# Kernel optimization log

Measured on AMD Instinct MI355X. Metric: run time of the kernel, lower is better.

Reference implementation:

```python
import jax, jax.numpy as jnp
import numpy as np

B, S, D, H = 2, 2048, 1024, 16
DK = D // H

def setup_inputs() -> dict:
    key = jax.random.key(0)
    ks = jax.random.split(key, 12)
    scale = 1.0 / np.sqrt(D)
    inp = {
        'q': jax.random.normal(ks[0], (B, S, D), jnp.float32),
        'k': jax.random.normal(ks[1], (B, S, D), jnp.float32),
        'v': jax.random.normal(ks[2], (B, S, D), jnp.float32),
        # causal mask: 1 where attending is allowed (j <= i), 0 for future tokens
        'mask': jnp.tril(jnp.ones((S, S), jnp.int32))[None, None, :, :],
        'wq': jax.random.normal(ks[3], (D, D), jnp.float32) * scale,
        'bq': jnp.zeros((D,), jnp.float32),
        'wk': jax.random.normal(ks[4], (D, D), jnp.float32) * scale,
        'bk': jnp.zeros((D,), jnp.float32),
        'wv': jax.random.normal(ks[5], (D, D), jnp.float32) * scale,
        'bv': jnp.zeros((D,), jnp.float32),
        'wo': jax.random.normal(ks[6], (D, D), jnp.float32) * scale,
        'bo': jnp.zeros((D,), jnp.float32),
    }
    return inp


def reference(q, k, v, mask, wq, bq, wk, bk, wv, bv, wo, bo):
    def split_heads(x):
        # [B,S,D] -> [B,H,S,DK]
        return x.reshape(B, S, H, DK).transpose(0, 2, 1, 3)

    query = split_heads(q @ wq + bq)
    key_ = split_heads(k @ wk + bk)
    value = split_heads(v @ wv + bv)

    # [B,H,S,S] attention scores
    scores = jnp.einsum('bhqd,bhkd->bhqk', query, key_) / jnp.sqrt(
        jnp.asarray(DK, jnp.float32))
    scores = jnp.where(mask == 0, jnp.asarray(-1e9, scores.dtype), scores)
    attn = jax.nn.softmax(scores, axis=-1)  # dropout p=0.0 (eval mode)

    x = jnp.einsum('bhqk,bhkd->bhqd', attn, value)  # [B,H,S,DK]
    x = x.transpose(0, 2, 1, 3).reshape(B, S, D)
    return x @ wo + bo
```

## Files before the change

### kernel.cpp

```cpp
#include <hip/hip_runtime.h>
#include <hip/hip_bf16.h>

#define BATCH 2
#define SEQ   2048
#define DMODEL 1024
#define NHEAD 16
#define DK    64
#define MTOK  (BATCH * SEQ)

typedef __attribute__((ext_vector_type(8))) short bf16x8;
typedef __attribute__((ext_vector_type(4))) float f32x4;

__device__ __forceinline__ unsigned short f2bf(float x) {
    unsigned u = __float_as_uint(x);
    u = (u + 0x7FFFu + ((u >> 16) & 1u)) >> 16;
    return (unsigned short)u;
}

__device__ __forceinline__ void store_out(float* p, float v)          { *p = v; }
__device__ __forceinline__ void store_out(unsigned short* p, float v) { *p = f2bf(v); }

__device__ __forceinline__ unsigned cvt_pk_bf16(float x, float y) {
    unsigned d;
    asm("v_cvt_pk_bf16_f32 %0, %1, %2" : "=v"(d) : "v"(x), "v"(y));
    return d;
}

__device__ __forceinline__ void g2lds16(const void* g, void* l) {
    __builtin_amdgcn_global_load_lds(
        (const __attribute__((address_space(1))) void*)g,
        (__attribute__((address_space(3))) void*)l, 16, 0, 0);
}

template <int N>
__device__ __forceinline__ void s_wait_vmcnt() {
    asm volatile("s_waitcnt vmcnt(%0)" :: "n"(N) : "memory");
}
__device__ __forceinline__ void s_wait_lgkm0() {
    asm volatile("s_waitcnt lgkmcnt(0)" ::: "memory");
}
__device__ __forceinline__ void s_bar() {
    asm volatile("s_barrier" ::: "memory");
}

__global__ __launch_bounds__(256) void cvt3_bf16_kernel(
    const float* __restrict__ s0, const float* __restrict__ s1,
    const float* __restrict__ s2,
    unsigned short* __restrict__ d0, unsigned short* __restrict__ d1,
    unsigned short* __restrict__ d2, int n)
{
    const float* src; unsigned short* dst;
    switch (blockIdx.z) {
        case 0:  src = s0; dst = d0; break;
        case 1:  src = s1; dst = d1; break;
        default: src = s2; dst = d2; break;
    }
    int i = (blockIdx.x * 256 + threadIdx.x) * 8;
    if (i >= n) return;
    float4 a = *(const float4*)(src + i);
    float4 b = *(const float4*)(src + i + 4);
    union { unsigned short s[8]; uint4 u; } o;
    o.s[0] = f2bf(a.x); o.s[1] = f2bf(a.y); o.s[2] = f2bf(a.z); o.s[3] = f2bf(a.w);
    o.s[4] = f2bf(b.x); o.s[5] = f2bf(b.y); o.s[6] = f2bf(b.z); o.s[7] = f2bf(b.w);
    *(uint4*)(dst + i) = o.u;
}

__global__ __launch_bounds__(256) void wtrans_kernel(
    const float* __restrict__ w0, const float* __restrict__ w1,
    const float* __restrict__ w2, const float* __restrict__ w3,
    unsigned short* __restrict__ t0, unsigned short* __restrict__ t1,
    unsigned short* __restrict__ t2, unsigned short* __restrict__ t3)
{
    __shared__ float tile[32][33];
    const float* W; unsigned short* T;
    switch (blockIdx.z) {
        case 0:  W = w0; T = t0; break;
        case 1:  W = w1; T = t1; break;
        case 2:  W = w2; T = t2; break;
        default: W = w3; T = t3; break;
    }
    const int n0 = blockIdx.x * 32, k0 = blockIdx.y * 32;
    const int t  = threadIdx.x;
    const int r  = t >> 3;
    const int c4 = (t & 7) * 4;

    float4 v = *(const float4*)&W[(size_t)(k0 + r) * DMODEL + n0 + c4];
    tile[r][c4 + 0] = v.x; tile[r][c4 + 1] = v.y;
    tile[r][c4 + 2] = v.z; tile[r][c4 + 3] = v.w;
    __syncthreads();

    union { unsigned short s[4]; uint2 u; } o;
#pragma unroll
    for (int u = 0; u < 4; ++u) o.s[u] = f2bf(tile[c4 + u][r]);
    *(uint2*)&T[(size_t)(n0 + r) * DMODEL + k0 + c4] = o.u;
}

struct GemmP {
    const unsigned short* A;
    const unsigned short* Bt;
    const float* bias;
    void* C;
    int N, K, ctShift, biasByRow;
    float scale;
};
struct Gemm3 { GemmP p[3]; };

template <typename OutT, int MR, int NC>
__global__ __launch_bounds__(512, 2) void gemm_lds_kernel(Gemm3 g)
{
    constexpr int AM    = MR / 2;
    constexpr int NCW   = NC / 4;
    constexpr int NBLK  = 2 * MR + 2 * NC;
    constexpr int PW    = NBLK / 8;
    constexpr int BUFSZ = NBLK * 512;

    __shared__ unsigned short sS[2 * BUFSZ];

    const unsigned nx  = gridDim.x;
    const unsigned lin = blockIdx.x + nx * blockIdx.z;
    const unsigned ch  = (nx * gridDim.z) >> 3;
    const unsigned l2  = (lin & 7u) * ch + (lin >> 3);
    const unsigned zz  = l2 / nx;
    const unsigned bid = l2 - zz * nx;

    const GemmP p = g.p[zz];
    const unsigned short* __restrict__ A  = p.A;
    const unsigned short* __restrict__ Bt = p.Bt;
    OutT* __restrict__ C = (OutT*)p.C;
    const int K = p.K, N = p.N;

    const int bx = (int)(bid & ((1u << p.ctShift) - 1u));
    const int by = (int)(bid >> p.ctShift);
    const int row0 = by * (MR * 16);
    const int col0 = bx * (NC * 16);

    const int t    = threadIdx.x;
    const int w    = t >> 6;
    const int lane = t & 63;
    const int ln   = lane & 15;
    const int qg   = lane >> 4;
    const int wm   = w >> 2;
    const int wn   = w & 3;

    const unsigned short* sp[PW];
    int lo[PW];
#pragma unroll
    for (int i = 0; i < PW; ++i) {
        const int s = w * PW + i;
        if (s < 2 * MR) {
            const int mtg = s >> 1, kc = s & 1;
            sp[i] = A + (size_t)(row0 + mtg * 16 + ln) * K + kc * 32 + qg * 8;
        } else {
            const int bi = s - 2 * MR;
            const int ntg = bi >> 1, kc = bi & 1;
            sp[i] = Bt + (size_t)(col0 + ntg * 16 + ln) * K + kc * 32 + qg * 8;
        }
        lo[i] = s * 512;
    }

    f32x4 acc[AM][NCW];
#pragma unroll
    for (int mt = 0; mt < AM; ++mt)
#pragma unroll
        for (int nt = 0; nt < NCW; ++nt) acc[mt][nt] = (f32x4){0.f, 0.f, 0.f, 0.f};

    const int NT = K / 64;

#pragma unroll
    for (int i = 0; i < PW; ++i) g2lds16(sp[i], &sS[lo[i]]);
#pragma unroll
    for (int i = 0; i < PW; ++i) g2lds16(sp[i] + 64, &sS[BUFSZ + lo[i]]);

    int curOff = 0;
    for (int kt = 0; kt < NT; ++kt) {
        if (kt < NT - 1) s_wait_vmcnt<PW>();
        else             s_wait_vmcnt<0>();
        s_bar();

        const unsigned short* bufA = &sS[curOff];
        const unsigned short* bufB = &sS[curOff + 2 * MR * 512];
#pragma unroll
        for (int kc = 0; kc < 2; ++kc) {
            bf16x8 aF[AM], bF[NCW];
#pragma unroll
            for (int mt = 0; mt < AM; ++mt)
                aF[mt] = *(const bf16x8*)&bufA[(((wm * AM + mt) * 2) + kc) * 512 + lane * 8];
#pragma unroll
            for (int n2 = 0; n2 < NCW; ++n2)
                bF[n2] = *(const bf16x8*)&bufB[(((wn * NCW + n2) * 2) + kc) * 512 + lane * 8];
#pragma unroll
            for (int mt = 0; mt < AM; ++mt)
#pragma unroll
                for (int n2 = 0; n2 < NCW; ++n2)
                    acc[mt][n2] = __builtin_amdgcn_mfma_f32_16x16x32_bf16(
                        aF[mt], bF[n2], acc[mt][n2], 0, 0, 0);
        }

        s_wait_lgkm0();
        s_bar();

        if (kt + 2 < NT) {
            const int koff = (kt + 2) * 64;
#pragma unroll
            for (int i = 0; i < PW; ++i)
                g2lds16(sp[i] + koff, &sS[curOff + lo[i]]);
        }
        curOff ^= BUFSZ;
    }

    float bcol[NCW], brow[AM][4];
    if (!p.biasByRow) {
#pragma unroll
        for (int n2 = 0; n2 < NCW; ++n2)
            bcol[n2] = p.bias[col0 + (wn * NCW + n2) * 16 + ln];
    } else {
#pragma unroll
        for (int mt = 0; mt < AM; ++mt)
#pragma unroll
            for (int r = 0; r < 4; ++r)
                brow[mt][r] = p.bias[row0 + wm * (AM * 16) + mt * 16 + qg * 4 + r];
    }

#pragma unroll
    for (int mt = 0; mt < AM; ++mt)
#pragma unroll
        for (int n2 = 0; n2 < NCW; ++n2)
#pragma unroll
            for (int r = 0; r < 4; ++r) {
                int row = row0 + wm * (AM * 16) + mt * 16 + qg * 4 + r;
                int col = col0 + (wn * NCW + n2) * 16 + ln;
                float bb = p.biasByRow ? brow[mt][r] : bcol[n2];
                store_out(&C[(size_t)row * N + col], (acc[mt][n2][r] + bb) * p.scale);
            }
}

#define BR 64
#define BC 64

__global__ __launch_bounds__(256) void attn_mfma_kernel(
    const unsigned short* __restrict__ Qg, const unsigned short* __restrict__ Kg,
    const unsigned short* __restrict__ VT, unsigned short* __restrict__ O)
{
    __shared__ unsigned short sK[2][8 * 512];
    __shared__ unsigned short sV[2][8 * 512];
    __shared__ unsigned short sQ[8 * 512];

    const int t    = threadIdx.x;
    const int w    = t >> 6;
    const int lane = t & 63;
    const int ln   = lane & 15;
    const int qg   = lane >> 4;

    const int id  = blockIdx.x;
    const int bh  = id & 31;
    const int qt  = (SEQ / BR - 1) - (id >> 5);
    const int b   = bh >> 4;
    const int h   = bh & 15;
    const int qi0 = qt * BR;

    const size_t rowbase = (size_t)b * SEQ;
    const size_t colbase = (size_t)h * DK;

#pragma unroll
    for (int i = 0; i < 2; ++i) {
        const int s = w * 2 + i;
        const int nt = s >> 1, kc = s & 1;
        g2lds16(Qg + (rowbase + qi0 + w * 16 + ln) * DMODEL + colbase + i * 32 + qg * 8,
                &sQ[s * 512]);
        g2lds16(Kg + (rowbase + nt * 16 + ln) * DMODEL + colbase + kc * 32 + qg * 8,
                &sK[0][s * 512]);
        g2lds16(VT + (size_t)(colbase + nt * 16 + ln) * MTOK + rowbase + kc * 32 + qg * 8,
                &sV[0][s * 512]);
    }
    __syncthreads();

    bf16x8 aq[2];
#pragma unroll
    for (int kc = 0; kc < 2; ++kc)
        aq[kc] = *(const bf16x8*)&sQ[(w * 2 + kc) * 512 + lane * 8];

    f32x4 ofrag[4];
#pragma unroll
    for (int nt = 0; nt < 4; ++nt) ofrag[nt] = (f32x4){0.f, 0.f, 0.f, 0.f};
    float osum_p = 0.f;
    float m_run  = -3.0e38f;

    const int laneA = ((2 * qg) & 3) * 16 + ln;
    const int laneB = ((2 * qg + 1) & 3) * 16 + ln;
    const bool hiSel = (qg >> 1) & 1;

    const int ntiles = qt + 1;
    for (int jt = 0; jt < ntiles; ++jt) {
        const int cur = jt & 1;

        if (jt + 1 < ntiles) {
            const int j1 = (jt + 1) * BC;
            const int nb = cur ^ 1;
#pragma unroll
            for (int i = 0; i < 2; ++i) {
                const int s = w * 2 + i;
                const int nt = s >> 1, kc = s & 1;
                g2lds16(Kg + (rowbase + j1 + nt * 16 + ln) * DMODEL + colbase + kc * 32 + qg * 8,
                        &sK[nb][s * 512]);
                g2lds16(VT + (size_t)(colbase + nt * 16 + ln) * MTOK + rowbase + j1 + kc * 32 + qg * 8,
                        &sV[nb][s * 512]);
            }
        }

        f32x4 sf[4];
#pragma unroll
        for (int nt = 0; nt < 4; ++nt) {
            f32x4 a2 = (f32x4){0.f, 0.f, 0.f, 0.f};
#pragma unroll
            for (int kc = 0; kc < 2; ++kc) {
                bf16x8 bk = *(const bf16x8*)&sK[cur][(nt * 2 + kc) * 512 + lane * 8];
                a2 = __builtin_amdgcn_mfma_f32_16x16x32_bf16(bk, aq[kc], a2, 0, 0, 0);
            }
            sf[nt] = a2;
        }

        if (jt == ntiles - 1) {
            const int qloc = w * 16 + ln;
#pragma unroll
            for (int nt = 0; nt < 4; ++nt)
#pragma unroll
                for (int r = 0; r < 4; ++r)
                    if (nt * 16 + qg * 4 + r > qloc) sf[nt][r] = -1.0e30f;
        }

        float pmax = sf[0][0];
#pragma unroll
        for (int nt = 0; nt < 4; ++nt)
#pragma unroll
            for (int r = 0; r < 4; ++r) pmax = fmaxf(pmax, sf[nt][r]);
        pmax = fmaxf(pmax, __shfl_xor(pmax, 16));
        pmax = fmaxf(pmax, __shfl_xor(pmax, 32));

        const float mn = fmaxf(m_run, pmax);
        const float al = exp2f(m_run - mn);
        m_run = mn;

        float pv[4][4];
        float lsum = 0.f;
#pragma unroll
        for (int nt = 0; nt < 4; ++nt)
#pragma unroll
            for (int r = 0; r < 4; ++r) {
                float e = exp2f(sf[nt][r] - mn);
                pv[nt][r] = e;
                lsum += e;
            }
        osum_p = osum_p * al + lsum;

        float alr[4];
#pragma unroll
        for (int r = 0; r < 4; ++r) alr[r] = __shfl(al, qg * 4 + r);
#pragma unroll
        for (int nt = 0; nt < 4; ++nt)
#pragma unroll
            for (int r = 0; r < 4; ++r) ofrag[nt][r] *= alr[r];

        unsigned pk0[2], pk1[2], pk2[2], pk3[2];
#pragma unroll
        for (int rr = 0; rr < 2; ++rr) {
            pk0[rr] = cvt_pk_bf16(pv[0][2 * rr], pv[0][2 * rr + 1]);
            pk1[rr] = cvt_pk_bf16(pv[1][2 * rr], pv[1][2 * rr + 1]);
            pk2[rr] = cvt_pk_bf16(pv[2][2 * rr], pv[2][2 * rr + 1]);
            pk3[rr] = cvt_pk_bf16(pv[3][2 * rr], pv[3][2 * rr + 1]);
        }
        union { bf16x8 v; unsigned u[4]; } ap[2];
        {
            unsigned s0, s1;
            s0 = (unsigned)__shfl((int)pk0[0], laneA); s1 = (unsigned)__shfl((int)pk1[0], laneA);
            ap[0].u[0] = hiSel ? s1 : s0;
            s0 = (unsigned)__shfl((int)pk0[1], laneA); s1 = (unsigned)__shfl((int)pk1[1], laneA);
            ap[0].u[1] = hiSel ? s1 : s0;
            s0 = (unsigned)__shfl((int)pk0[0], laneB); s1 = (unsigned)__shfl((int)pk1[0], laneB);
            ap[0].u[2] = hiSel ? s1 : s0;
            s0 = (unsigned)__shfl((int)pk0[1], laneB); s1 = (unsigned)__shfl((int)pk1[1], laneB);
            ap[0].u[3] = hiSel ? s1 : s0;
            s0 = (unsigned)__shfl((int)pk2[0], laneA); s1 = (unsigned)__shfl((int)pk3[0], laneA);
            ap[1].u[0] = hiSel ? s1 : s0;
            s0 = (unsigned)__shfl((int)pk2[1], laneA); s1 = (unsigned)__shfl((int)pk3[1], laneA);
            ap[1].u[1] = hiSel ? s1 : s0;
            s0 = (unsigned)__shfl((int)pk2[0], laneB); s1 = (unsigned)__shfl((int)pk3[0], laneB);
            ap[1].u[2] = hiSel ? s1 : s0;
            s0 = (unsigned)__shfl((int)pk2[1], laneB); s1 = (unsigned)__shfl((int)pk3[1], laneB);
            ap[1].u[3] = hiSel ? s1 : s0;
        }

#pragma unroll
        for (int nt = 0; nt < 4; ++nt) {
#pragma unroll
            for (int kc = 0; kc < 2; ++kc) {
                bf16x8 bv = *(const bf16x8*)&sV[cur][(nt * 2 + kc) * 512 + lane * 8];
                ofrag[nt] = __builtin_amdgcn_mfma_f32_16x16x32_bf16(ap[kc].v, bv, ofrag[nt], 0, 0, 0);
            }
        }

        __syncthreads();
    }

    float osum = osum_p + __shfl_xor(osum_p, 16);
    osum += __shfl_xor(osum, 32);
    const float invq = 1.0f / osum;
    float inv[4];
#pragma unroll
    for (int r = 0; r < 4; ++r) inv[r] = __shfl(invq, qg * 4 + r);
#pragma unroll
    for (int nt = 0; nt < 4; ++nt)
#pragma unroll
        for (int r = 0; r < 4; ++r) {
            int gq = qi0 + w * 16 + qg * 4 + r;
            O[(rowbase + gq) * DMODEL + colbase + nt * 16 + ln] =
                f2bf(ofrag[nt][r] * inv[r]);
        }
}

extern "C" void kernel_launch(void* const* d_in, const int* in_sizes, int n_in,
                              void* d_out, int out_size, void* d_ws, size_t ws_size,
                              hipStream_t stream)
{
    const float* q  = (const float*)d_in[0];
    const float* k  = (const float*)d_in[1];
    const float* v  = (const float*)d_in[2];
    const float* wq = (const float*)d_in[4];
    const float* bq = (const float*)d_in[5];
    const float* wk = (const float*)d_in[6];
    const float* bk = (const float*)d_in[7];
    const float* wv = (const float*)d_in[8];
    const float* bv = (const float*)d_in[9];
    const float* wo = (const float*)d_in[10];
    const float* bo = (const float*)d_in[11];
    float* out = (float*)d_out;

    const size_t mat  = (size_t)MTOK * DMODEL;
    const size_t wmat = (size_t)DMODEL * DMODEL;
    unsigned short* Abq = (unsigned short*)d_ws;
    unsigned short* Abk = Abq + mat;
    unsigned short* Abv = Abk + mat;
    unsigned short* WtQ = Abv + mat;
    unsigned short* WtK = WtQ + wmat;
    unsigned short* WtV = WtK + wmat;
    unsigned short* WtO = WtV + wmat;
    unsigned short* Qb  = WtO + wmat;
    unsigned short* Kb  = Qb + mat;
    unsigned short* VT  = Kb + mat;
    unsigned short* CTX = VT + mat;

    cvt3_bf16_kernel<<<dim3((unsigned)(mat / 2048), 1, 3), 256, 0, stream>>>(
        q, k, v, Abq, Abk, Abv, (int)mat);
    wtrans_kernel<<<dim3(32, 32, 4), 256, 0, stream>>>(wq, wk, wv, wo, WtQ, WtK, WtV, WtO);

    const float qscale = 0.125f * 1.44269504088896f;
    Gemm3 g;
    g.p[0] = (GemmP){Abq, WtQ, bq, (void*)Qb, DMODEL, DMODEL, 2, 0, qscale};
    g.p[1] = (GemmP){Abk, WtK, bk, (void*)Kb, DMODEL, DMODEL, 2, 0, 1.0f};
    g.p[2] = (GemmP){WtV, Abv, bv, (void*)VT, MTOK,   DMODEL, 4, 1, 1.0f};
    gemm_lds_kernel<unsigned short, 16, 16><<<dim3(64, 1, 3), 512, 0, stream>>>(g);

    attn_mfma_kernel<<<BATCH * NHEAD * (SEQ / BR), 256, 0, stream>>>(Qb, Kb, VT, CTX);

    Gemm3 go;
    go.p[0] = (GemmP){CTX, WtO, bo, (void*)out, DMODEL, DMODEL, 3, 0, 1.0f};
    go.p[1] = go.p[0];
    go.p[2] = go.p[0];
    gemm_lds_kernel<float, 8, 8><<<dim3(256, 1, 1), 512, 0, stream>>>(go);
}
```

Measured before the change: 257.1 us.

## Pipeline GEMM at half-tile (k=32) granularity with four-stage prefetch and MFMA priority

The GEMM main loop now advances in k=32 half-steps instead of k=64. Each half-slot of the double buffer is refilled as soon as it is consumed, so four half-tiles are in flight and the graduated vmcnt waits allow finer overlap of global-to-LDS loads with MFMA work. It also raises wave priority around the MFMA block with s_setprio. The cost is twice as many barriers per K and smaller compute chunks between them, which may offset the gain from better latency hiding.

```diff
diff --git a/kernel.cpp b/kernel.cpp
--- a/kernel.cpp
+++ b/kernel.cpp
@@ -110,9 +110,8 @@
 {
     constexpr int AM    = MR / 2;
     constexpr int NCW   = NC / 4;
-    constexpr int NBLK  = 2 * MR + 2 * NC;
-    constexpr int PW    = NBLK / 8;
-    constexpr int BUFSZ = NBLK * 512;
+    constexpr int HL    = (MR + NC) / 8;
+    constexpr int BUFSZ = (2 * MR + 2 * NC) * 512;
 
     __shared__ unsigned short sS[2 * BUFSZ];
 
@@ -142,20 +141,21 @@
     const int wm   = w >> 2;
     const int wn   = w & 3;
 
-    const unsigned short* sp[PW];
-    int lo[PW];
-#pragma unroll
-    for (int i = 0; i < PW; ++i) {
-        const int s = w * PW + i;
-        if (s < 2 * MR) {
-            const int mtg = s >> 1, kc = s & 1;
-            sp[i] = A + (size_t)(row0 + mtg * 16 + ln) * K + kc * 32 + qg * 8;
+    const unsigned short* sp[HL];
+    int d0[HL];
+    int dk[HL];
+#pragma unroll
+    for (int i = 0; i < HL; ++i) {
+        const int j = w * HL + i;
+        if (j < MR) {
+            sp[i] = A + (size_t)(row0 + j * 16 + ln) * K + qg * 8;
+            d0[i] = j * 512;
+            dk[i] = MR * 512;
         } else {
-            const int bi = s - 2 * MR;
-            const int ntg = bi >> 1, kc = bi & 1;
-            sp[i] = Bt + (size_t)(col0 + ntg * 16 + ln) * K + kc * 32 + qg * 8;
-        }
-        lo[i] = s * 512;
+            sp[i] = Bt + (size_t)(col0 + (j - MR) * 16 + ln) * K + qg * 8;
+            d0[i] = (2 * MR + (j - MR)) * 512;
+            dk[i] = NC * 512;
+        }
     }
 
     f32x4 acc[AM][NCW];
@@ -164,48 +164,54 @@
 #pragma unroll
         for (int nt = 0; nt < NCW; ++nt) acc[mt][nt] = (f32x4){0.f, 0.f, 0.f, 0.f};
 
-    const int NT = K / 64;
-
-#pragma unroll
-    for (int i = 0; i < PW; ++i) g2lds16(sp[i], &sS[lo[i]]);
-#pragma unroll
-    for (int i = 0; i < PW; ++i) g2lds16(sp[i] + 64, &sS[BUFSZ + lo[i]]);
-
-    int curOff = 0;
-    for (int kt = 0; kt < NT; ++kt) {
-        if (kt < NT - 1) s_wait_vmcnt<PW>();
-        else             s_wait_vmcnt<0>();
+    const int NH = K / 32;
+
+#pragma unroll
+    for (int hh = 0; hh < 4; ++hh) {
+        const int hb = (hh & 2) ? BUFSZ : 0;
+        const int kc = hh & 1;
+#pragma unroll
+        for (int i = 0; i < HL; ++i)
+            g2lds16(sp[i] + hh * 32, &sS[hb + d0[i] + kc * dk[i]]);
+    }
+
+    for (int h = 0; h < NH; ++h) {
+        if      (h + 3 < NH) s_wait_vmcnt<3 * HL>();
+        else if (h + 2 < NH) s_wait_vmcnt<2 * HL>();
+        else if (h + 1 < NH) s_wait_vmcnt<1 * HL>();
+        else                 s_wait_vmcnt<0>();
         s_bar();
 
-        const unsigned short* bufA = &sS[curOff];
-        const unsigned short* bufB = &sS[curOff + 2 * MR * 512];
-#pragma unroll
-        for (int kc = 0; kc < 2; ++kc) {
-            bf16x8 aF[AM], bF[NCW];
-#pragma unroll
-            for (int mt = 0; mt < AM; ++mt)
-                aF[mt] = *(const bf16x8*)&bufA[(((wm * AM + mt) * 2) + kc) * 512 + lane * 8];
+        const int hb = (h & 2) ? BUFSZ : 0;
+        const int kc = h & 1;
+        const unsigned short* bufA = &sS[hb + kc * (MR * 512)];
+        const unsigned short* bufB = &sS[hb + 2 * MR * 512 + kc * (NC * 512)];
+
+        bf16x8 aF[AM], bF[NCW];
+#pragma unroll
+        for (int mt = 0; mt < AM; ++mt)
+            aF[mt] = *(const bf16x8*)&bufA[(wm * AM + mt) * 512 + lane * 8];
+#pragma unroll
+        for (int n2 = 0; n2 < NCW; ++n2)
+            bF[n2] = *(const bf16x8*)&bufB[(wn * NCW + n2) * 512 + lane * 8];
+
+        __builtin_amdgcn_s_setprio(1);
+#pragma unroll
+        for (int mt = 0; mt < AM; ++mt)
 #pragma unroll
             for (int n2 = 0; n2 < NCW; ++n2)
-                bF[n2] = *(const bf16x8*)&bufB[(((wn * NCW + n2) * 2) + kc) * 512 + lane * 8];
-#pragma unroll
-            for (int mt = 0; mt < AM; ++mt)
-#pragma unroll
-                for (int n2 = 0; n2 < NCW; ++n2)
-                    acc[mt][n2] = __builtin_amdgcn_mfma_f32_16x16x32_bf16(
-                        aF[mt], bF[n2], acc[mt][n2], 0, 0, 0);
-        }
+                acc[mt][n2] = __builtin_amdgcn_mfma_f32_16x16x32_bf16(
+                    aF[mt], bF[n2], acc[mt][n2], 0, 0, 0);
+        __builtin_amdgcn_s_setprio(0);
 
         s_wait_lgkm0();
         s_bar();
 
-        if (kt + 2 < NT) {
-            const int koff = (kt + 2) * 64;
-#pragma unroll
-            for (int i = 0; i < PW; ++i)
-                g2lds16(sp[i] + koff, &sS[curOff + lo[i]]);
-        }
-        curOff ^= BUFSZ;
+        if (h + 4 < NH) {
+#pragma unroll
+            for (int i = 0; i < HL; ++i)
+                g2lds16(sp[i] + (h + 4) * 32, &sS[hb + d0[i] + kc * dk[i]]);
+        }
     }
 
     float bcol[NCW], brow[AM][4];
```

Measured after the change: 256.4 us. Within noise of the previous version (-0.2%).

## Split GEMM main loop into quadrant phases with barriers and MFMA priority

Applied to the files above, without the earlier changes.

Reworks the LDS-staged GEMM K-loop into four quadrant sub-phases (A-lo/B-lo, A-lo/B-hi, A-hi/B-lo, A-hi/B-hi). Fragment loads from LDS are interleaved with MFMA bursts, and the MFMA bursts are fenced by workgroup barriers and raised wave priority. The global prefetch moves from two tiles ahead to one tile ahead, issued at the start of each iteration, with a full vmcnt wait at the end. The aim is to overlap LDS reads with matrix math across waves in a ping-pong style. In exchange it adds many barriers and gives less lookahead to hide global-load latency.

```diff
diff --git a/kernel.cpp b/kernel.cpp
--- a/kernel.cpp
+++ b/kernel.cpp
@@ -110,6 +110,8 @@
 {
     constexpr int AM    = MR / 2;
     constexpr int NCW   = NC / 4;
+    constexpr int AMH   = AM / 2;
+    constexpr int NCWH  = NCW / 2;
     constexpr int NBLK  = 2 * MR + 2 * NC;
     constexpr int PW    = NBLK / 8;
     constexpr int BUFSZ = NBLK * 512;
@@ -168,44 +170,100 @@
 
 #pragma unroll
     for (int i = 0; i < PW; ++i) g2lds16(sp[i], &sS[lo[i]]);
-#pragma unroll
-    for (int i = 0; i < PW; ++i) g2lds16(sp[i] + 64, &sS[BUFSZ + lo[i]]);
-
-    int curOff = 0;
+    s_wait_vmcnt<0>();
+    s_bar();
+
     for (int kt = 0; kt < NT; ++kt) {
-        if (kt < NT - 1) s_wait_vmcnt<PW>();
-        else             s_wait_vmcnt<0>();
-        s_bar();
-
-        const unsigned short* bufA = &sS[curOff];
-        const unsigned short* bufB = &sS[curOff + 2 * MR * 512];
-#pragma unroll
-        for (int kc = 0; kc < 2; ++kc) {
-            bf16x8 aF[AM], bF[NCW];
-#pragma unroll
-            for (int mt = 0; mt < AM; ++mt)
-                aF[mt] = *(const bf16x8*)&bufA[(((wm * AM + mt) * 2) + kc) * 512 + lane * 8];
-#pragma unroll
-            for (int n2 = 0; n2 < NCW; ++n2)
-                bF[n2] = *(const bf16x8*)&bufB[(((wn * NCW + n2) * 2) + kc) * 512 + lane * 8];
-#pragma unroll
-            for (int mt = 0; mt < AM; ++mt)
-#pragma unroll
-                for (int n2 = 0; n2 < NCW; ++n2)
+        const int boff = (kt & 1) ? BUFSZ : 0;
+        const unsigned short* bufA = &sS[boff];
+        const unsigned short* bufB = &sS[boff + 2 * MR * 512];
+
+        bf16x8 aLo[AMH][2], aHi[AMH][2], bLo[NCWH][2], bHi[NCWH][2];
+
+        if (kt + 1 < NT) {
+            const int koff = (kt + 1) * 64;
+            const int doff = boff ^ BUFSZ;
+#pragma unroll
+            for (int i = 0; i < PW; ++i)
+                g2lds16(sp[i] + koff, &sS[doff + lo[i]]);
+        }
+#pragma unroll
+        for (int mt = 0; mt < AMH; ++mt)
+#pragma unroll
+            for (int kc = 0; kc < 2; ++kc)
+                aLo[mt][kc] = *(const bf16x8*)&bufA[((wm * AM + mt) * 2 + kc) * 512 + lane * 8];
+#pragma unroll
+        for (int n2 = 0; n2 < NCWH; ++n2)
+#pragma unroll
+            for (int kc = 0; kc < 2; ++kc)
+                bLo[n2][kc] = *(const bf16x8*)&bufB[((wn * NCW + n2) * 2 + kc) * 512 + lane * 8];
+        s_bar();
+        s_wait_lgkm0();
+        __builtin_amdgcn_sched_barrier(0);
+        __builtin_amdgcn_s_setprio(1);
+#pragma unroll
+        for (int mt = 0; mt < AMH; ++mt)
+#pragma unroll
+            for (int n2 = 0; n2 < NCWH; ++n2)
+#pragma unroll
+                for (int kc = 0; kc < 2; ++kc)
                     acc[mt][n2] = __builtin_amdgcn_mfma_f32_16x16x32_bf16(
-                        aF[mt], bF[n2], acc[mt][n2], 0, 0, 0);
-        }
-
+                        aLo[mt][kc], bLo[n2][kc], acc[mt][n2], 0, 0, 0);
+        __builtin_amdgcn_s_setprio(0);
+        s_bar();
+
+#pragma unroll
+        for (int n2 = 0; n2 < NCWH; ++n2)
+#pragma unroll
+            for (int kc = 0; kc < 2; ++kc)
+                bHi[n2][kc] = *(const bf16x8*)&bufB[((wn * NCW + NCWH + n2) * 2 + kc) * 512 + lane * 8];
+        s_bar();
         s_wait_lgkm0();
-        s_bar();
-
-        if (kt + 2 < NT) {
-            const int koff = (kt + 2) * 64;
-#pragma unroll
-            for (int i = 0; i < PW; ++i)
-                g2lds16(sp[i] + koff, &sS[curOff + lo[i]]);
-        }
-        curOff ^= BUFSZ;
+        __builtin_amdgcn_sched_barrier(0);
+        __builtin_amdgcn_s_setprio(1);
+#pragma unroll
+        for (int mt = 0; mt < AMH; ++mt)
+#pragma unroll
+            for (int n2 = 0; n2 < NCWH; ++n2)
+#pragma unroll
+                for (int kc = 0; kc < 2; ++kc)
+                    acc[mt][NCWH + n2] = __builtin_amdgcn_mfma_f32_16x16x32_bf16(
+                        aLo[mt][kc], bHi[n2][kc], acc[mt][NCWH + n2], 0, 0, 0);
+        __builtin_amdgcn_s_setprio(0);
+        s_bar();
+
+#pragma unroll
+        for (int mt = 0; mt < AMH; ++mt)
+#pragma unroll
+            for (int kc = 0; kc < 2; ++kc)
+                aHi[mt][kc] = *(const bf16x8*)&bufA[((wm * AM + AMH + mt) * 2 + kc) * 512 + lane * 8];
+        s_bar();
+        s_wait_lgkm0();
+        __builtin_amdgcn_sched_barrier(0);
+        __builtin_amdgcn_s_setprio(1);
+#pragma unroll
+        for (int mt = 0; mt < AMH; ++mt)
+#pragma unroll
+            for (int n2 = 0; n2 < NCWH; ++n2)
+#pragma unroll
+                for (int kc = 0; kc < 2; ++kc)
+                    acc[AMH + mt][n2] = __builtin_amdgcn_mfma_f32_16x16x32_bf16(
+                        aHi[mt][kc], bLo[n2][kc], acc[AMH + mt][n2], 0, 0, 0);
+        __builtin_amdgcn_s_setprio(0);
+        s_bar();
+
+        __builtin_amdgcn_s_setprio(1);
+#pragma unroll
+        for (int mt = 0; mt < AMH; ++mt)
+#pragma unroll
+            for (int n2 = 0; n2 < NCWH; ++n2)
+#pragma unroll
+                for (int kc = 0; kc < 2; ++kc)
+                    acc[AMH + mt][NCWH + n2] = __builtin_amdgcn_mfma_f32_16x16x32_bf16(
+                        aHi[mt][kc], bHi[n2][kc], acc[AMH + mt][NCWH + n2], 0, 0, 0);
+        __builtin_amdgcn_s_setprio(0);
+        s_wait_vmcnt<0>();
+        s_bar();
     }
 
     float bcol[NCW], brow[AM][4];
```

Result: slower. 266.3 us (+3.6%).

## Fuse fp32-to-bf16 activation conversion into QKV GEMM load pipeline

Applied to the files above, without the earlier changes.

Removes the separate cvt3 kernel that converted q/k/v activations to bf16 in workspace. The QKV GEMM now loads the fp32 activation tiles straight into registers, converts them with v_cvt_pk_bf16, and writes them to LDS, while the bf16 weight tiles still arrive by direct global-to-LDS loads. This avoids a full write and re-read of three activation matrices plus a kernel launch. In exchange the GEMM reads twice as many bytes for the A side, adds register pressure, and places a vmcnt wait and conversion step in the main loop. It also adds s_setprio around the MFMA block.

```diff
diff --git a/kernel.cpp b/kernel.cpp
--- a/kernel.cpp
+++ b/kernel.cpp
@@ -41,28 +41,6 @@
 }
 __device__ __forceinline__ void s_bar() {
     asm volatile("s_barrier" ::: "memory");
-}
-
-__global__ __launch_bounds__(256) void cvt3_bf16_kernel(
-    const float* __restrict__ s0, const float* __restrict__ s1,
-    const float* __restrict__ s2,
-    unsigned short* __restrict__ d0, unsigned short* __restrict__ d1,
-    unsigned short* __restrict__ d2, int n)
-{
-    const float* src; unsigned short* dst;
-    switch (blockIdx.z) {
-        case 0:  src = s0; dst = d0; break;
-        case 1:  src = s1; dst = d1; break;
-        default: src = s2; dst = d2; break;
-    }
-    int i = (blockIdx.x * 256 + threadIdx.x) * 8;
-    if (i >= n) return;
-    float4 a = *(const float4*)(src + i);
-    float4 b = *(const float4*)(src + i + 4);
-    union { unsigned short s[8]; uint4 u; } o;
-    o.s[0] = f2bf(a.x); o.s[1] = f2bf(a.y); o.s[2] = f2bf(a.z); o.s[3] = f2bf(a.w);
-    o.s[4] = f2bf(b.x); o.s[5] = f2bf(b.y); o.s[6] = f2bf(b.z); o.s[7] = f2bf(b.w);
-    *(uint4*)(dst + i) = o.u;
 }
 
 __global__ __launch_bounds__(256) void wtrans_kernel(
@@ -98,20 +76,24 @@
 struct GemmP {
     const unsigned short* A;
     const unsigned short* Bt;
+    const float* A32;
+    const float* B32;
     const float* bias;
     void* C;
-    int N, K, ctShift, biasByRow;
+    int N, K, ctShift, biasByRow, aF32, bF32;
     float scale;
 };
 struct Gemm3 { GemmP p[3]; };
 
-template <typename OutT, int MR, int NC>
-__global__ __launch_bounds__(512, 2) void gemm_lds_kernel(Gemm3 g)
+template <typename OutT, int MR, int NC, bool HASF32>
+__device__ __forceinline__ void gemm_body(const Gemm3& g)
 {
     constexpr int AM    = MR / 2;
     constexpr int NCW   = NC / 4;
     constexpr int NBLK  = 2 * MR + 2 * NC;
     constexpr int PW    = NBLK / 8;
+    constexpr int NF    = HASF32 ? PW / 2 : 0;
+    constexpr int NG    = PW - NF;
     constexpr int BUFSZ = NBLK * 512;
 
     __shared__ unsigned short sS[2 * BUFSZ];
@@ -124,8 +106,6 @@
     const unsigned bid = l2 - zz * nx;
 
     const GemmP p = g.p[zz];
-    const unsigned short* __restrict__ A  = p.A;
-    const unsigned short* __restrict__ Bt = p.Bt;
     OutT* __restrict__ C = (OutT*)p.C;
     const int K = p.K, N = p.N;
 
@@ -142,21 +122,43 @@
     const int wm   = w >> 2;
     const int wn   = w & 3;
 
-    const unsigned short* sp[PW];
-    int lo[PW];
-#pragma unroll
-    for (int i = 0; i < PW; ++i) {
-        const int s = w * PW + i;
+    const bool aF = HASF32 && (p.aF32 != 0);
+
+    const unsigned short* spG[NG];
+    int loG[NG];
+#pragma unroll
+    for (int j = 0; j < NG; ++j) {
+        const int i = HASF32 ? (aF ? NF + j : j) : j;
+        const int s = i * 8 + w;
         if (s < 2 * MR) {
             const int mtg = s >> 1, kc = s & 1;
-            sp[i] = A + (size_t)(row0 + mtg * 16 + ln) * K + kc * 32 + qg * 8;
+            spG[j] = p.A + (size_t)(row0 + mtg * 16 + ln) * K + kc * 32 + qg * 8;
         } else {
-            const int bi = s - 2 * MR;
-            const int ntg = bi >> 1, kc = bi & 1;
-            sp[i] = Bt + (size_t)(col0 + ntg * 16 + ln) * K + kc * 32 + qg * 8;
-        }
-        lo[i] = s * 512;
-    }
+            const int bi = s - 2 * MR, ntg = bi >> 1, kc = bi & 1;
+            spG[j] = p.Bt + (size_t)(col0 + ntg * 16 + ln) * K + kc * 32 + qg * 8;
+        }
+        loG[j] = s * 512;
+    }
+
+    const float* spF[NF > 0 ? NF : 1];
+    int loF[NF > 0 ? NF : 1];
+    if constexpr (HASF32) {
+#pragma unroll
+        for (int j = 0; j < NF; ++j) {
+            const int i = aF ? j : NF + j;
+            const int s = i * 8 + w;
+            if (s < 2 * MR) {
+                const int mtg = s >> 1, kc = s & 1;
+                spF[j] = p.A32 + (size_t)(row0 + mtg * 16 + ln) * K + kc * 32 + qg * 8;
+            } else {
+                const int bi = s - 2 * MR, ntg = bi >> 1, kc = bi & 1;
+                spF[j] = p.B32 + (size_t)(col0 + ntg * 16 + ln) * K + kc * 32 + qg * 8;
+            }
+            loF[j] = s * 512;
+        }
+    }
+
+    float4 rA[NF > 0 ? NF : 1], rB[NF > 0 ? NF : 1];
 
     f32x4 acc[AM][NCW];
 #pragma unroll
@@ -166,34 +168,68 @@
 
     const int NT = K / 64;
 
-#pragma unroll
-    for (int i = 0; i < PW; ++i) g2lds16(sp[i], &sS[lo[i]]);
-#pragma unroll
-    for (int i = 0; i < PW; ++i) g2lds16(sp[i] + 64, &sS[BUFSZ + lo[i]]);
-
-    int curOff = 0;
+    auto issueF = [&](int koff) {
+        if constexpr (HASF32) {
+#pragma unroll
+            for (int j = 0; j < NF; ++j) {
+                rA[j] = *(const float4*)(spF[j] + koff);
+                rB[j] = *(const float4*)(spF[j] + koff + 4);
+            }
+        }
+    };
+    auto issueG = [&](int koff, int dstOff) {
+#pragma unroll
+        for (int j = 0; j < NG; ++j)
+            g2lds16(spG[j] + koff, &sS[dstOff + loG[j]]);
+    };
+    auto cvtWrite = [&](int dstOff) {
+        if constexpr (HASF32) {
+#pragma unroll
+            for (int j = 0; j < NF; ++j) {
+                uint4 o;
+                o.x = cvt_pk_bf16(rA[j].x, rA[j].y);
+                o.y = cvt_pk_bf16(rA[j].z, rA[j].w);
+                o.z = cvt_pk_bf16(rB[j].x, rB[j].y);
+                o.w = cvt_pk_bf16(rB[j].z, rB[j].w);
+                *(uint4*)&sS[dstOff + loF[j] + lane * 8] = o;
+            }
+        }
+    };
+
+    issueF(0);
+    __builtin_amdgcn_sched_barrier(0);
+    issueG(0, 0);
+    cvtWrite(0);
+    issueF(64);
+    __builtin_amdgcn_sched_barrier(0);
+    issueG(64, BUFSZ);
+    cvtWrite(BUFSZ);
+    s_wait_vmcnt<4>();
+    s_wait_lgkm0();
+    s_bar();
+
     for (int kt = 0; kt < NT; ++kt) {
-        if (kt < NT - 1) s_wait_vmcnt<PW>();
-        else             s_wait_vmcnt<0>();
-        s_bar();
-
-        const unsigned short* bufA = &sS[curOff];
-        const unsigned short* bufB = &sS[curOff + 2 * MR * 512];
+        const int boff = (kt & 1) ? BUFSZ : 0;
+        const unsigned short* bufA = &sS[boff];
+        const unsigned short* bufB = &sS[boff + 2 * MR * 512];
+
 #pragma unroll
         for (int kc = 0; kc < 2; ++kc) {
-            bf16x8 aF[AM], bF[NCW];
+            bf16x8 aFr[AM], bFr[NCW];
 #pragma unroll
             for (int mt = 0; mt < AM; ++mt)
-                aF[mt] = *(const bf16x8*)&bufA[(((wm * AM + mt) * 2) + kc) * 512 + lane * 8];
+                aFr[mt] = *(const bf16x8*)&bufA[((wm * AM + mt) * 2 + kc) * 512 + lane * 8];
 #pragma unroll
             for (int n2 = 0; n2 < NCW; ++n2)
-                bF[n2] = *(const bf16x8*)&bufB[(((wn * NCW + n2) * 2) + kc) * 512 + lane * 8];
+                bFr[n2] = *(const bf16x8*)&bufB[((wn * NCW + n2) * 2 + kc) * 512 + lane * 8];
+            __builtin_amdgcn_s_setprio(1);
 #pragma unroll
             for (int mt = 0; mt < AM; ++mt)
 #pragma unroll
                 for (int n2 = 0; n2 < NCW; ++n2)
                     acc[mt][n2] = __builtin_amdgcn_mfma_f32_16x16x32_bf16(
-                        aF[mt], bF[n2], acc[mt][n2], 0, 0, 0);
+                        aFr[mt], bFr[n2], acc[mt][n2], 0, 0, 0);
+            __builtin_amdgcn_s_setprio(0);
         }
 
         s_wait_lgkm0();
@@ -201,11 +237,16 @@
 
         if (kt + 2 < NT) {
             const int koff = (kt + 2) * 64;
-#pragma unroll
-            for (int i = 0; i < PW; ++i)
-                g2lds16(sp[i] + koff, &sS[curOff + lo[i]]);
-        }
-        curOff ^= BUFSZ;
+            issueF(koff);
+            __builtin_amdgcn_sched_barrier(0);
+            issueG(koff, boff);
+            __builtin_amdgcn_sched_barrier(0);
+            s_wait_vmcnt<4>();
+            cvtWrite(boff);
+        } else {
+            s_wait_vmcnt<0>();
+        }
+        s_bar();
     }
 
     float bcol[NCW], brow[AM][4];
@@ -232,6 +273,15 @@
                 float bb = p.biasByRow ? brow[mt][r] : bcol[n2];
                 store_out(&C[(size_t)row * N + col], (acc[mt][n2][r] + bb) * p.scale);
             }
+}
+
+__global__ __launch_bounds__(512, 2) void gemm_qkv_kernel(Gemm3 g)
+{
+    gemm_body<unsigned short, 16, 16, true>(g);
+}
+__global__ __launch_bounds__(512, 2) void gemm_out_kernel(Gemm3 g)
+{
+    gemm_body<float, 8, 8, false>(g);
 }
 
 #define BR 64
@@ -436,10 +486,7 @@
 
     const size_t mat  = (size_t)MTOK * DMODEL;
     const size_t wmat = (size_t)DMODEL * DMODEL;
-    unsigned short* Abq = (unsigned short*)d_ws;
-    unsigned short* Abk = Abq + mat;
-    unsigned short* Abv = Abk + mat;
-    unsigned short* WtQ = Abv + mat;
+    unsigned short* WtQ = (unsigned short*)d_ws;
     unsigned short* WtK = WtQ + wmat;
     unsigned short* WtV = WtK + wmat;
     unsigned short* WtO = WtV + wmat;
@@ -448,22 +495,24 @@
     unsigned short* VT  = Kb + mat;
     unsigned short* CTX = VT + mat;
 
-    cvt3_bf16_kernel<<<dim3((unsigned)(mat / 2048), 1, 3), 256, 0, stream>>>(
-        q, k, v, Abq, Abk, Abv, (int)mat);
     wtrans_kernel<<<dim3(32, 32, 4), 256, 0, stream>>>(wq, wk, wv, wo, WtQ, WtK, WtV, WtO);
 
     const float qscale = 0.125f * 1.44269504088896f;
     Gemm3 g;
-    g.p[0] = (GemmP){Abq, WtQ, bq, (void*)Qb, DMODEL, DMODEL, 2, 0, qscale};
-    g.p[1] = (GemmP){Abk, WtK, bk, (void*)Kb, DMODEL, DMODEL, 2, 0, 1.0f};
-    g.p[2] = (GemmP){WtV, Abv, bv, (void*)VT, MTOK,   DMODEL, 4, 1, 1.0f};
-    gemm_lds_kernel<unsigned short, 16, 16><<<dim3(64, 1, 3), 512, 0, stream>>>(g);
+    g.p[0] = (GemmP){nullptr, WtQ, q, nullptr, bq, (void*)Qb,
+                     DMODEL, DMODEL, 2, 0, 1, 0, qscale};
+    g.p[1] = (GemmP){nullptr, WtK, k, nullptr, bk, (void*)Kb,
+                     DMODEL, DMODEL, 2, 0, 1, 0, 1.0f};
+    g.p[2] = (GemmP){WtV, nullptr, nullptr, v, bv, (void*)VT,
+                     MTOK, DMODEL, 4, 1, 0, 1, 1.0f};
+    gemm_qkv_kernel<<<dim3(64, 1, 3), 512, 0, stream>>>(g);
 
     attn_mfma_kernel<<<BATCH * NHEAD * (SEQ / BR), 256, 0, stream>>>(Qb, Kb, VT, CTX);
 
     Gemm3 go;
-    go.p[0] = (GemmP){CTX, WtO, bo, (void*)out, DMODEL, DMODEL, 3, 0, 1.0f};
+    go.p[0] = (GemmP){CTX, WtO, nullptr, nullptr, bo, (void*)out,
+                      DMODEL, DMODEL, 3, 0, 0, 0, 1.0f};
     go.p[1] = go.p[0];
     go.p[2] = go.p[0];
-    gemm_lds_kernel<float, 8, 8><<<dim3(256, 1, 1), 512, 0, stream>>>(go);
-}
+    gemm_out_kernel<<<dim3(256, 1, 1), 512, 0, stream>>>(go);
+}
```

Result: slower. 283.1 us (+10.1%).
